# Kernel optimization log

Hardware: AMD Instinct MI355X
Metric: run time of the kernel (lower is better)

Reference implementation:

```python
import jax, jax.numpy as jnp
import numpy as np

N = 8_000_000  # number of (parent, child, relation) edges
N_RELS = 64
P = 3  # n_polarities


def sparsemax(z):
    # sparsemax along last axis (Martins & Astudillo 2016)
    d = z.shape[-1]
    zs = jnp.sort(z, axis=-1)[..., ::-1]          # descending
    cs = jnp.cumsum(zs, axis=-1)
    k = jnp.arange(1, d + 1, dtype=z.dtype)
    support = 1.0 + k * zs > cs                   # [.., d] bool
    ksup = jnp.sum(support, axis=-1, keepdims=True)  # int, size of support
    tau = (jnp.take_along_axis(cs, ksup - 1, axis=-1) - 1.0) / ksup.astype(z.dtype)
    return jnp.maximum(z - tau, 0.0)


def setup_inputs() -> dict:
    key = jax.random.key(0)
    k1, k2, k3, k4, k5 = jax.random.split(key, 5)
    prnt_probs = jax.random.uniform(k1, (N, P), dtype=jnp.float32)
    child_probs = jax.random.uniform(k2, (N, P), dtype=jnp.float32)
    rels = jax.random.randint(k3, (N,), 0, N_RELS, dtype=jnp.int32)
    # learned params (torch inits to ones/constants; perturb so grads are non-degenerate)
    M = 1.0 + 0.1 * jax.random.normal(k4, (N_RELS, P, P), dtype=jnp.float32)
    beta = jax.random.uniform(k5, (N_RELS, P), dtype=jnp.float32)
    z_epsilon = jnp.float32(0.01)
    scale_factor = jnp.float32(21.0)
    return {"prnt_probs": prnt_probs, "child_probs": child_probs, "M": M,
            "beta": beta, "z_epsilon": z_epsilon, "scale_factor": scale_factor,
            "rels": rels, "var_sfx": 0}


def reference(prnt_probs, child_probs, M, beta, z_epsilon, scale_factor, rels, var_sfx):
    # All rows of child_probs/prnt_probs are nonzero (uniform fill), so the
    # nonzero() gathers select every edge and the copy branch is empty:
    # this is the dense alpha path of AlphaModel.forward.
    c = jnp.einsum('nij,nj->ni', M[rels], child_probs)  # relation-gated bmm
    c = sparsemax(c)
    c = sparsemax(c)  # alpha branch re-applies sparsemax (idempotent but faithful)
    p = sparsemax(prnt_probs)
    b = beta[rels]
    alpha = (1.0 - b) * p + b * c
    # scale(): entropy of clamped mixture + cosine similarity
    z = jnp.maximum(p + c, jax.lax.stop_gradient(z_epsilon))  # torch uses .item() -> no grad
    z = z / jnp.sum(z, axis=-1, keepdims=True)
    entropy = -jnp.sum(z * jnp.log(z), axis=-1)
    cos = jnp.sum(p * c, axis=-1)
    norm = jnp.maximum(jnp.linalg.norm(p, axis=-1) * jnp.linalg.norm(c, axis=-1), 1e-10)
    cos = 0.1 + cos / norm
    scale = scale_factor * cos / entropy
    alpha = jnp.maximum(alpha * scale[:, None], 0.001)
    return alpha
```

## Files before the change

### kernel.cpp

```cpp
#include <hip/hip_runtime.h>

#define NRELS 64
#define BLOCK 256

__device__ __forceinline__ float fast_ln(float x) {
    return 0.69314718056f * __builtin_amdgcn_logf(x);
}
__device__ __forceinline__ float fast_rcp(float x) {
    return __builtin_amdgcn_rcpf(x);
}
__device__ __forceinline__ float fast_rsq(float x) {
    return __builtin_amdgcn_rsqf(x);
}

__device__ __forceinline__ void sparsemax3(float z0, float z1, float z2,
                                           float& o0, float& o1, float& o2) {
    float lo01 = fminf(z0, z1), hi01 = fmaxf(z0, z1);
    float s2 = fminf(lo01, z2);
    float mx = fmaxf(lo01, z2);
    float s0 = fmaxf(hi01, mx);
    float s1 = fminf(hi01, mx);
    float cs2 = s0 + s1;
    float cs3 = cs2 + s2;
    bool k2 = (1.0f + 2.0f * s1 > cs2);
    bool k3 = (1.0f + 3.0f * s2 > cs3);
    int k = 1 + (int)k2 + (int)k3;
    float csk = (k == 1) ? s0 : ((k == 2) ? cs2 : cs3);
    float rk  = (k == 1) ? 1.0f : ((k == 2) ? 0.5f : 0.33333334f);
    float tau = (csk - 1.0f) * rk;
    o0 = fmaxf(z0 - tau, 0.0f);
    o1 = fmaxf(z1 - tau, 0.0f);
    o2 = fmaxf(z2 - tau, 0.0f);
}

__device__ __forceinline__ void edge_compute(
    float p0, float p1, float p2,
    float q0, float q1, float q2,
    int r, const float* sM, const float* sB,
    float zeps, float sf,
    float& a0o, float& a1o, float& a2o) {
    const float4 ma = *(const float4*)&sM[r * 12];
    const float4 mb = *(const float4*)&sM[r * 12 + 4];
    const float  m22 = sM[r * 12 + 8];
    float c0 = ma.x * q0 + ma.y * q1 + ma.z * q2;
    float c1 = ma.w * q0 + mb.x * q1 + mb.y * q2;
    float c2 = mb.z * q0 + mb.w * q1 + m22 * q2;
    sparsemax3(c0, c1, c2, c0, c1, c2);
    sparsemax3(c0, c1, c2, c0, c1, c2);
    sparsemax3(p0, p1, p2, p0, p1, p2);
    const float4 bv = *(const float4*)&sB[r * 4];
    float a0 = (1.0f - bv.x) * p0 + bv.x * c0;
    float a1 = (1.0f - bv.y) * p1 + bv.y * c1;
    float a2 = (1.0f - bv.z) * p2 + bv.z * c2;
    float z0 = fmaxf(p0 + c0, zeps);
    float z1 = fmaxf(p1 + c1, zeps);
    float z2 = fmaxf(p2 + c2, zeps);
    float rs = fast_rcp(z0 + z1 + z2);
    z0 *= rs; z1 *= rs; z2 *= rs;
    float ent = -(z0 * fast_ln(z0) + z1 * fast_ln(z1) + z2 * fast_ln(z2));
    float dot = p0 * c0 + p1 * c1 + p2 * c2;
    float pp = p0 * p0 + p1 * p1 + p2 * p2;
    float cc = c0 * c0 + c1 * c1 + c2 * c2;
    float cosv = 0.1f + dot * fast_rsq(fmaxf(pp * cc, 1e-20f));
    float scale = sf * cosv * fast_rcp(ent);
    a0o = fmaxf(a0 * scale, 0.001f);
    a1o = fmaxf(a1 * scale, 0.001f);
    a2o = fmaxf(a2 * scale, 0.001f);
}

__global__ __launch_bounds__(BLOCK) void alpha_kernel(
    const float* __restrict__ prnt, const float* __restrict__ child,
    const float* __restrict__ Mg, const float* __restrict__ betag,
    const float* __restrict__ zeps_p, const float* __restrict__ sf_p,
    const int* __restrict__ rels, float* __restrict__ out, int n_edges) {
    __shared__ __align__(16) float sM[NRELS * 12];
    __shared__ __align__(16) float sB[NRELS * 4];
    for (int i = threadIdx.x; i < NRELS * 9; i += BLOCK) {
        int r = i / 9, rem = i - r * 9;
        sM[r * 12 + rem] = Mg[i];
    }
    for (int i = threadIdx.x; i < NRELS * 3; i += BLOCK) {
        int r = i / 3, rem = i - r * 3;
        sB[r * 4 + rem] = betag[i];
    }
    __syncthreads();

    const float zeps = zeps_p[0];
    const float sf   = sf_p[0];
    const int nt4 = n_edges >> 2;
    int t = blockIdx.x * BLOCK + threadIdx.x;

    if (t < nt4) {
        const float4* p4 = (const float4*)prnt;
        const float4* c4 = (const float4*)child;
        float4* o4 = (float4*)out;
        int4 r4 = ((const int4*)rels)[t];
        float4 pa = p4[3 * t + 0], pb = p4[3 * t + 1], pc = p4[3 * t + 2];
        float4 ca = c4[3 * t + 0], cb = c4[3 * t + 1], cc = c4[3 * t + 2];
        float P[12] = {pa.x, pa.y, pa.z, pa.w, pb.x, pb.y, pb.z, pb.w,
                       pc.x, pc.y, pc.z, pc.w};
        float C[12] = {ca.x, ca.y, ca.z, ca.w, cb.x, cb.y, cb.z, cb.w,
                       cc.x, cc.y, cc.z, cc.w};
        int R[4] = {r4.x, r4.y, r4.z, r4.w};
        float O[12];
        #pragma unroll
        for (int e = 0; e < 4; e++) {
            edge_compute(P[3 * e], P[3 * e + 1], P[3 * e + 2],
                         C[3 * e], C[3 * e + 1], C[3 * e + 2],
                         R[e], sM, sB, zeps, sf,
                         O[3 * e], O[3 * e + 1], O[3 * e + 2]);
        }
        float4 oa = {O[0], O[1], O[2],  O[3]};
        float4 ob = {O[4], O[5], O[6],  O[7]};
        float4 oc = {O[8], O[9], O[10], O[11]};
        o4[3 * t + 0] = oa;
        o4[3 * t + 1] = ob;
        o4[3 * t + 2] = oc;
    } else if (t == nt4) {
        for (int e = nt4 * 4; e < n_edges; e++) {
            float a0, a1, a2;
            edge_compute(prnt[3 * e], prnt[3 * e + 1], prnt[3 * e + 2],
                         child[3 * e], child[3 * e + 1], child[3 * e + 2],
                         rels[e], sM, sB, zeps, sf, a0, a1, a2);
            out[3 * e] = a0; out[3 * e + 1] = a1; out[3 * e + 2] = a2;
        }
    }
}

extern "C" void kernel_launch(void* const* d_in, const int* in_sizes, int n_in,
                              void* d_out, int out_size, void* d_ws, size_t ws_size,
                              hipStream_t stream) {
    const float* prnt  = (const float*)d_in[0];
    const float* child = (const float*)d_in[1];
    const float* Mg    = (const float*)d_in[2];
    const float* betag = (const float*)d_in[3];
    const float* zeps  = (const float*)d_in[4];
    const float* sf    = (const float*)d_in[5];
    const int*   rels  = (const int*)d_in[6];
    float* out = (float*)d_out;

    int n_edges = in_sizes[0] / 3;
    int nthreads = (n_edges >> 2) + 1;
    int nblocks = (nthreads + BLOCK - 1) / BLOCK;
    alpha_kernel<<<nblocks, BLOCK, 0, stream>>>(
        prnt, child, Mg, betag, zeps, sf, rels, out, n_edges);
}
```

Baseline: 264.8 us.

## Stage prnt/child/out through shared memory for coalesced float4 global access

After: 267.6 us. No clear change (+1.1%).

```diff
diff --git a/kernel.cpp b/kernel.cpp
--- a/kernel.cpp
+++ b/kernel.cpp
@@ -2,6 +2,7 @@
 
 #define NRELS 64
 #define BLOCK 256
+#define EPB   1024
 
 __device__ __forceinline__ float fast_ln(float x) {
     return 0.69314718056f * __builtin_amdgcn_logf(x);
@@ -75,6 +76,9 @@
     const int* __restrict__ rels, float* __restrict__ out, int n_edges) {
     __shared__ __align__(16) float sM[NRELS * 12];
     __shared__ __align__(16) float sB[NRELS * 4];
+    __shared__ __align__(16) float sP[EPB * 3];
+    __shared__ __align__(16) float sC[EPB * 3];
+
     for (int i = threadIdx.x; i < NRELS * 9; i += BLOCK) {
         int r = i / 9, rem = i - r * 9;
         sM[r * 12 + rem] = Mg[i];
@@ -83,20 +87,34 @@
         int r = i / 3, rem = i - r * 3;
         sB[r * 4 + rem] = betag[i];
     }
-    __syncthreads();
 
     const float zeps = zeps_p[0];
     const float sf   = sf_p[0];
-    const int nt4 = n_edges >> 2;
-    int t = blockIdx.x * BLOCK + threadIdx.x;
+    const int e0 = blockIdx.x * EPB;
+    const int n  = min(EPB, n_edges - e0);
+    const long base_f = (long)e0 * 3;
+    const int t = threadIdx.x;
 
-    if (t < nt4) {
-        const float4* p4 = (const float4*)prnt;
-        const float4* c4 = (const float4*)child;
-        float4* o4 = (float4*)out;
-        int4 r4 = ((const int4*)rels)[t];
-        float4 pa = p4[3 * t + 0], pb = p4[3 * t + 1], pc = p4[3 * t + 2];
-        float4 ca = c4[3 * t + 0], cb = c4[3 * t + 1], cc = c4[3 * t + 2];
+    if (n == EPB) {
+        const float4* pg = (const float4*)(prnt + base_f);
+        const float4* cg = (const float4*)(child + base_f);
+        float4* sp4 = (float4*)sP;
+        float4* sc4 = (float4*)sC;
+        #pragma unroll
+        for (int s = 0; s < 3; s++) {
+            int idx = t + s * BLOCK;
+            sp4[idx] = pg[idx];
+            sc4[idx] = cg[idx];
+        }
+        int4 r4 = ((const int4*)rels)[(e0 >> 2) + t];
+        __syncthreads();
+
+        const float4* pf = (const float4*)(sP + 12 * t);
+        const float4* cf = (const float4*)(sC + 12 * t);
+        float4 pa = pf[0], pb = pf[1], pc = pf[2];
+        float4 ca = cf[0], cb = cf[1], cc = cf[2];
+        __syncthreads();
+
         float P[12] = {pa.x, pa.y, pa.z, pa.w, pb.x, pb.y, pb.z, pb.w,
                        pc.x, pc.y, pc.z, pc.w};
         float C[12] = {ca.x, ca.y, ca.z, ca.w, cb.x, cb.y, cb.z, cb.w,
@@ -110,19 +128,33 @@
                          R[e], sM, sB, zeps, sf,
                          O[3 * e], O[3 * e + 1], O[3 * e + 2]);
         }
-        float4 oa = {O[0], O[1], O[2],  O[3]};
-        float4 ob = {O[4], O[5], O[6],  O[7]};
-        float4 oc = {O[8], O[9], O[10], O[11]};
-        o4[3 * t + 0] = oa;
-        o4[3 * t + 1] = ob;
-        o4[3 * t + 2] = oc;
-    } else if (t == nt4) {
-        for (int e = nt4 * 4; e < n_edges; e++) {
+
+        float4* of = (float4*)(sP + 12 * t);
+        of[0] = (float4){O[0], O[1], O[2],  O[3]};
+        of[1] = (float4){O[4], O[5], O[6],  O[7]};
+        of[2] = (float4){O[8], O[9], O[10], O[11]};
+        __syncthreads();
+
+        float4* og = (float4*)(out + base_f);
+        #pragma unroll
+        for (int s = 0; s < 3; s++) {
+            int idx = t + s * BLOCK;
+            og[idx] = sp4[idx];
+        }
+    } else {
+        for (int f = t; f < n * 3; f += BLOCK) {
+            sP[f] = prnt[base_f + f];
+            sC[f] = child[base_f + f];
+        }
+        __syncthreads();
+        for (int e = 4 * t; e < min(4 * t + 4, n); e++) {
             float a0, a1, a2;
-            edge_compute(prnt[3 * e], prnt[3 * e + 1], prnt[3 * e + 2],
-                         child[3 * e], child[3 * e + 1], child[3 * e + 2],
-                         rels[e], sM, sB, zeps, sf, a0, a1, a2);
-            out[3 * e] = a0; out[3 * e + 1] = a1; out[3 * e + 2] = a2;
+            edge_compute(sP[3 * e], sP[3 * e + 1], sP[3 * e + 2],
+                         sC[3 * e], sC[3 * e + 1], sC[3 * e + 2],
+                         rels[e0 + e], sM, sB, zeps, sf, a0, a1, a2);
+            out[base_f + 3 * e]     = a0;
+            out[base_f + 3 * e + 1] = a1;
+            out[base_f + 3 * e + 2] = a2;
         }
     }
 }
@@ -140,8 +172,7 @@
     float* out = (float*)d_out;
 
     int n_edges = in_sizes[0] / 3;
-    int nthreads = (n_edges >> 2) + 1;
-    int nblocks = (nthreads + BLOCK - 1) / BLOCK;
+    int nblocks = (n_edges + EPB - 1) / EPB;
     alpha_kernel<<<nblocks, BLOCK, 0, stream>>>(
         prnt, child, Mg, betag, zeps, sf, rels, out, n_edges);
 }
```
